# Kernel tuning notes

Measured on AMD Instinct MI355X. Metric: run time of the kernel, lower is better.

The kernel has to match this reference:

```python
import jax, jax.numpy as jnp
import numpy as np
import math

B, S, D = 4, 2048, 1024
WINDOW = 10  # window_size; attends to |i-j| <= WINDOW//2


def setup_inputs() -> dict:
    key = jax.random.key(0)
    ks = jax.random.split(key, 9)
    sc = 1.0 / math.sqrt(D)
    return {
        "x": jax.random.normal(ks[0], (B, S, D), dtype=jnp.float32),
        "Wq": jax.random.normal(ks[1], (D, D), dtype=jnp.float32) * sc,
        "bq": jnp.zeros((D,), dtype=jnp.float32),
        "Wk": jax.random.normal(ks[2], (D, D), dtype=jnp.float32) * sc,
        "bk": jnp.zeros((D,), dtype=jnp.float32),
        "Wv": jax.random.normal(ks[3], (D, D), dtype=jnp.float32) * sc,
        "bv": jnp.zeros((D,), dtype=jnp.float32),
        "Wo": jax.random.normal(ks[4], (D, D), dtype=jnp.float32) * sc,
        "bo": jnp.zeros((D,), dtype=jnp.float32),
    }


def _local_mask(seq_len: int, window_size: int) -> jnp.ndarray:
    # row i attends to columns [i - w//2, i + w//2] inclusive -> |i - j| <= w//2
    i = jnp.arange(seq_len)[:, None]
    j = jnp.arange(seq_len)[None, :]
    return jnp.abs(i - j) <= (window_size // 2)  # [S, S] bool


def reference(x, Wq, bq, Wk, bk, Wv, bv, Wo, bo):
    # nn.Linear: y = x @ W.T + b
    Q = x @ Wq.T + bq  # [B, S, D]
    K = x @ Wk.T + bk
    V = x @ Wv.T + bv
    scores = jnp.einsum("bqd,bkd->bqk", Q, K) / jnp.float32(math.sqrt(D))
    mask = _local_mask(x.shape[1], WINDOW)
    scores = jnp.where(mask[None, :, :], scores, jnp.float32(-1e9))
    attn = jax.nn.softmax(scores, axis=-1)  # [B, S, S]
    context = jnp.einsum("bqk,bkd->bqd", attn, V)
    output = context @ Wo.T + bo
    return output, attn
```

## Files before the change

### kernel.cpp

```cpp
#include <hip/hip_runtime.h>
#include <hip/hip_bf16.h>
#include <cstdint>
#include <cstddef>


typedef __attribute__((ext_vector_type(8))) short bf16x8;
typedef __attribute__((ext_vector_type(4))) float f32x4;
typedef __attribute__((ext_vector_type(8))) unsigned short ushortx8;

#define GPTR(x) ((const __attribute__((address_space(1))) void*)(x))
#define LPTR(x) ((__attribute__((address_space(3))) void*)(x))

__device__ __forceinline__ unsigned short f2bf(float f) {
    __hip_bfloat16 h = __float2bfloat16(f);
    unsigned short u;
    __builtin_memcpy(&u, &h, 2);
    return u;
}
__device__ __forceinline__ float bf2f(unsigned short u) {
    unsigned int x = ((unsigned int)u) << 16;
    float f;
    __builtin_memcpy(&f, &x, 4);
    return f;
}

__global__ void cvt_all(const float* __restrict__ x,
                        const float* __restrict__ Wq, const float* __restrict__ Wk,
                        const float* __restrict__ Wv, const float* __restrict__ Wo,
                        unsigned short* __restrict__ xh,
                        unsigned short* __restrict__ Wcat,
                        unsigned short* __restrict__ Woh) {
    const int idx = blockIdx.x * blockDim.x + threadIdx.x;
    const float* src;
    unsigned short* dst;
    int s_off, d_off;
    if (idx < 2097152) {
        src = x; dst = xh; s_off = idx; d_off = idx;
    } else {
        const int r   = idx - 2097152;
        const int seg = r >> 18;
        const int off = r & 262143;
        src   = (seg == 0) ? Wq : (seg == 1) ? Wk : (seg == 2) ? Wv : Wo;
        dst   = (seg < 3) ? Wcat : Woh;
        s_off = off;
        d_off = (seg < 3) ? (seg << 18) + off : off;
    }
    f32x4 v = reinterpret_cast<const f32x4*>(src)[s_off];
    ushort4 o;
    o.x = f2bf(v[0]); o.y = f2bf(v[1]); o.z = f2bf(v[2]); o.w = f2bf(v[3]);
    reinterpret_cast<ushort4*>(dst)[d_off] = o;
}

__device__ __forceinline__ void gemm_core(const unsigned short* __restrict__ A,
                                          const unsigned short* __restrict__ Bw,
                                          int K, int tm, int tn,
                                          unsigned short* As, unsigned short* Bs,
                                          f32x4 (&acc)[4][4]) {
    const int tid  = threadIdx.x;
    const int lane = tid & 63;
    const int w    = tid >> 6;
    const int wr   = w >> 1;
    const int wc   = w & 1;

    const int lrow8 = lane >> 3;
    const int lcolb = (lane & 7) << 4;

    const char* Abase = (const char*)(A + (size_t)tm * 128 * (size_t)K);
    const char* Bbase = (const char*)(Bw + (size_t)tn * 128 * (size_t)K);
    const size_t rstride = (size_t)K * 2;

    const int nk = K >> 6;
    for (int t = 0; t < nk; ++t) {
        const size_t k0b = ((size_t)t << 6) * 2;
#pragma unroll
        for (int ii = 0; ii < 4; ++ii) {
            const int c    = (w << 2) + ii;
            const int row  = (c << 3) + lrow8;
            const int csrc = lcolb ^ ((row & 7) << 4);
            __builtin_amdgcn_global_load_lds(
                GPTR(Abase + (size_t)row * rstride + k0b + (size_t)csrc),
                LPTR((char*)As + (c << 10)), 16, 0, 0);
            __builtin_amdgcn_global_load_lds(
                GPTR(Bbase + (size_t)row * rstride + k0b + (size_t)csrc),
                LPTR((char*)Bs + (c << 10)), 16, 0, 0);
        }
        __syncthreads();

#pragma unroll
        for (int kk = 0; kk < 2; ++kk) {
            bf16x8 af[4], bfr[4];
            const int cb = (kk << 6) + ((lane >> 4) << 4);
#pragma unroll
            for (int m = 0; m < 4; ++m) {
                const int row = (wr << 6) + (m << 4) + (lane & 15);
                af[m] = *reinterpret_cast<const bf16x8*>(
                    (const char*)As + row * 128 + (cb ^ ((row & 7) << 4)));
            }
#pragma unroll
            for (int n = 0; n < 4; ++n) {
                const int row = (wc << 6) + (n << 4) + (lane & 15);
                bfr[n] = *reinterpret_cast<const bf16x8*>(
                    (const char*)Bs + row * 128 + (cb ^ ((row & 7) << 4)));
            }
#pragma unroll
            for (int m = 0; m < 4; ++m)
#pragma unroll
                for (int n = 0; n < 4; ++n)
                    acc[m][n] = __builtin_amdgcn_mfma_f32_16x16x32_bf16(
                        af[m], bfr[n], acc[m][n], 0, 0, 0);
        }
        __syncthreads();
    }
}

__launch_bounds__(256, 3)
__global__ void gemm_qkv(const unsigned short* __restrict__ A,
                         const unsigned short* __restrict__ Bw,
                         const float* __restrict__ bq, const float* __restrict__ bk,
                         const float* __restrict__ bv,
                         unsigned short* __restrict__ C, int M, int N, int K) {
    __shared__ unsigned short As[128 * 64];
    __shared__ unsigned short Bs[128 * 64];
    f32x4 acc[4][4];
#pragma unroll
    for (int m = 0; m < 4; ++m)
#pragma unroll
        for (int n = 0; n < 4; ++n) acc[m][n] = (f32x4){0.f, 0.f, 0.f, 0.f};

    const int ntn = N >> 7;
    const int sid = (blockIdx.x & 7) * (gridDim.x >> 3) + (blockIdx.x >> 3);
    const int tm  = sid / ntn;
    const int tn  = sid % ntn;

    gemm_core(A, Bw, K, tm, tn, As, Bs, acc);

    const int lane = threadIdx.x & 63;
    const int w    = threadIdx.x >> 6;
    const int wr   = w >> 1, wc = w & 1;
    const int seg  = tn >> 3;
    const float* bp = (seg == 0) ? bq : (seg == 1) ? bk : bv;

    const int col0 = (tn << 7) + (wc << 6) + (lane & 15);
    const int row0 = (tm << 7) + (wr << 6) + ((lane >> 4) << 2);
#pragma unroll
    for (int n = 0; n < 4; ++n) {
        const int col = col0 + (n << 4);
        const float bb = bp[col & 1023];
#pragma unroll
        for (int m = 0; m < 4; ++m) {
            const int row = row0 + (m << 4);
#pragma unroll
            for (int r = 0; r < 4; ++r)
                C[(size_t)(row + r) * (size_t)N + col] = f2bf(acc[m][n][r] + bb);
        }
    }
}

__launch_bounds__(256, 3)
__global__ void gemm_out(const unsigned short* __restrict__ A,
                         const unsigned short* __restrict__ Bw,
                         const float* __restrict__ bias,
                         float* __restrict__ C, int M, int N, int K) {
    __shared__ unsigned short As[128 * 64];
    __shared__ unsigned short Bs[128 * 64];
    f32x4 acc[4][4];
#pragma unroll
    for (int m = 0; m < 4; ++m)
#pragma unroll
        for (int n = 0; n < 4; ++n) acc[m][n] = (f32x4){0.f, 0.f, 0.f, 0.f};

    const int sid = (blockIdx.x & 7) * (gridDim.x >> 3) + (blockIdx.x >> 3);
    const int tm  = sid >> 3;
    const int tn  = sid & 7;

    gemm_core(A, Bw, K, tm, tn, As, Bs, acc);

    const int lane = threadIdx.x & 63;
    const int w    = threadIdx.x >> 6;
    const int wr   = w >> 1, wc = w & 1;
    const int col0 = (tn << 7) + (wc << 6) + (lane & 15);
    const int row0 = (tm << 7) + (wr << 6) + ((lane >> 4) << 2);
#pragma unroll
    for (int n = 0; n < 4; ++n) {
        const int col = col0 + (n << 4);
        const float bb = bias[col];
#pragma unroll
        for (int m = 0; m < 4; ++m) {
            const int row = row0 + (m << 4);
#pragma unroll
            for (int r = 0; r < 4; ++r)
                C[(size_t)(row + r) * (size_t)N + col] = acc[m][n][r] + bb;
        }
    }
}

__launch_bounds__(256, 4)
__global__ void attn_band_kernel(const unsigned short* __restrict__ QKV,
                                 float* __restrict__ attn,
                                 unsigned short* __restrict__ ctx) {
    __shared__ float psm[4][16];
    const int bid  = blockIdx.x;
    const int rb   = (bid & 7) * 256 + (bid >> 3);
    const int w    = threadIdx.x >> 6;
    const int lane = threadIdx.x & 63;
    const int g    = (rb << 2) + w;
    const int b    = g >> 11;
    const int i    = g & 2047;

    const unsigned short* qrow = QKV + (size_t)g * 3072;
    float qf[16];
    {
        ushortx8 qa = *reinterpret_cast<const ushortx8*>(qrow + (lane << 4));
        ushortx8 qb = *reinterpret_cast<const ushortx8*>(qrow + (lane << 4) + 8);
#pragma unroll
        for (int t = 0; t < 8; ++t) { qf[t] = bf2f(qa[t]); qf[8 + t] = bf2f(qb[t]); }
    }

    float s[11];
#pragma unroll
    for (int jj = 0; jj < 11; ++jj) {
        const int j = i - 5 + jj;
        const bool valid = ((unsigned)j < 2048u);
        const int jc = min(max(j, 0), 2047);
        const unsigned short* krow = QKV + ((size_t)(b << 11) + jc) * 3072 + 1024;
        ushortx8 ka = *reinterpret_cast<const ushortx8*>(krow + (lane << 4));
        ushortx8 kb = *reinterpret_cast<const ushortx8*>(krow + (lane << 4) + 8);
        float d = 0.f;
#pragma unroll
        for (int t = 0; t < 8; ++t)
            d += qf[t] * bf2f(ka[t]) + qf[8 + t] * bf2f(kb[t]);
#pragma unroll
        for (int off = 32; off >= 1; off >>= 1) d += __shfl_xor(d, off, 64);
        s[jj] = valid ? d * 0.03125f : -1e30f;
    }

    float mx = s[0];
#pragma unroll
    for (int jj = 1; jj < 11; ++jj) mx = fmaxf(mx, s[jj]);
    float p[11], sum = 0.f;
#pragma unroll
    for (int jj = 0; jj < 11; ++jj) { p[jj] = expf(s[jj] - mx); sum += p[jj]; }
    const float inv = 1.0f / sum;

    if (lane == 0) {
#pragma unroll
        for (int jj = 0; jj < 11; ++jj) psm[w][jj] = p[jj] * inv;
    }
    __syncthreads();

    const int lo = i - 5;
    float* arow = attn + (size_t)g * 2048;
#pragma unroll
    for (int e = 0; e < 8; ++e) {
        const int c0 = (e << 8) + (lane << 2);
        f32x4 v = (f32x4){0.f, 0.f, 0.f, 0.f};
        if (c0 + 3 >= lo && c0 <= lo + 10) {
#pragma unroll
            for (int t = 0; t < 4; ++t) {
                const int d = c0 + t - lo;
                if ((unsigned)d < 11u) v[t] = psm[w][d];
            }
        }
        *reinterpret_cast<f32x4*>(arow + c0) = v;
    }

    float cacc[16];
#pragma unroll
    for (int t = 0; t < 16; ++t) cacc[t] = 0.f;
#pragma unroll
    for (int jj = 0; jj < 11; ++jj) {
        const int j  = i - 5 + jj;
        const int jc = min(max(j, 0), 2047);
        const float pj = p[jj] * inv;
        const unsigned short* vrow = QKV + ((size_t)(b << 11) + jc) * 3072 + 2048;
        ushortx8 va = *reinterpret_cast<const ushortx8*>(vrow + (lane << 4));
        ushortx8 vb = *reinterpret_cast<const ushortx8*>(vrow + (lane << 4) + 8);
#pragma unroll
        for (int t = 0; t < 8; ++t) {
            cacc[t]     += pj * bf2f(va[t]);
            cacc[8 + t] += pj * bf2f(vb[t]);
        }
    }
    unsigned short* cp = ctx + (size_t)g * 1024 + (lane << 4);
    ushortx8 oa, ob;
#pragma unroll
    for (int t = 0; t < 8; ++t) { oa[t] = f2bf(cacc[t]); ob[t] = f2bf(cacc[8 + t]); }
    *reinterpret_cast<ushortx8*>(cp)     = oa;
    *reinterpret_cast<ushortx8*>(cp + 8) = ob;
}

extern "C" void kernel_launch(void* const* d_in, const int* in_sizes, int n_in,
                              void* d_out, int out_size, void* d_ws, size_t ws_size,
                              hipStream_t stream) {
    const float* x  = (const float*)d_in[0];
    const float* Wq = (const float*)d_in[1];
    const float* bq = (const float*)d_in[2];
    const float* Wk = (const float*)d_in[3];
    const float* bk = (const float*)d_in[4];
    const float* Wv = (const float*)d_in[5];
    const float* bv = (const float*)d_in[6];
    const float* Wo = (const float*)d_in[7];
    const float* bo = (const float*)d_in[8];

    const size_t MS = 8192, DD = 1024;

    float* out  = (float*)d_out;
    float* attn = out + MS * DD;

    char* ws = (char*)d_ws;
    unsigned short* xh   = (unsigned short*)ws; ws += MS * DD * 2;
    unsigned short* Wcat = (unsigned short*)ws; ws += 3 * DD * DD * 2;
    unsigned short* Woh  = (unsigned short*)ws; ws += DD * DD * 2;
    unsigned short* QKV  = (unsigned short*)ws; ws += MS * 3 * DD * 2;
    unsigned short* ctx  = (unsigned short*)ws; ws += MS * DD * 2;

    cvt_all<<<dim3(12288), dim3(256), 0, stream>>>(x, Wq, Wk, Wv, Wo, xh, Wcat, Woh);

    gemm_qkv<<<dim3(1536), dim3(256), 0, stream>>>(xh, Wcat, bq, bk, bv,
                                                   QKV, 8192, 3072, 1024);

    attn_band_kernel<<<dim3(2048), dim3(256), 0, stream>>>(QKV, attn, ctx);

    gemm_out<<<dim3(512), dim3(256), 0, stream>>>(ctx, Woh, bo, out, 8192, 1024, 1024);
}
```

Baseline: 136.8 us.

## Fold output projection into V weights by precomputing Wo·Wv

```diff
diff --git a/kernel.cpp b/kernel.cpp
--- a/kernel.cpp
+++ b/kernel.cpp
@@ -26,7 +26,7 @@
 
 __global__ void cvt_all(const float* __restrict__ x,
                         const float* __restrict__ Wq, const float* __restrict__ Wk,
-                        const float* __restrict__ Wv, const float* __restrict__ Wo,
+                        const float* __restrict__ Wo,
                         unsigned short* __restrict__ xh,
                         unsigned short* __restrict__ Wcat,
                         unsigned short* __restrict__ Woh) {
@@ -40,15 +40,50 @@
         const int r   = idx - 2097152;
         const int seg = r >> 18;
         const int off = r & 262143;
-        src   = (seg == 0) ? Wq : (seg == 1) ? Wk : (seg == 2) ? Wv : Wo;
-        dst   = (seg < 3) ? Wcat : Woh;
+        src   = (seg == 0) ? Wq : (seg == 1) ? Wk : Wo;
+        dst   = (seg < 2) ? Wcat : Woh;
         s_off = off;
-        d_off = (seg < 3) ? (seg << 18) + off : off;
+        d_off = (seg < 2) ? (seg << 18) + off : off;
     }
     f32x4 v = reinterpret_cast<const f32x4*>(src)[s_off];
     ushort4 o;
     o.x = f2bf(v[0]); o.y = f2bf(v[1]); o.z = f2bf(v[2]); o.w = f2bf(v[3]);
     reinterpret_cast<ushort4*>(dst)[d_off] = o;
+}
+
+__global__ void transpose_cvt(const float* __restrict__ in,
+                              unsigned short* __restrict__ out) {
+    __shared__ float tl[64][65];
+    const int t  = threadIdx.x;
+    const int c  = t & 63;
+    const int r4 = t >> 6;
+    const int bx = blockIdx.x;
+    const int by = blockIdx.y;
+#pragma unroll
+    for (int i = 0; i < 16; ++i) {
+        const int r = r4 * 16 + i;
+        tl[r][c] = in[(size_t)(by * 64 + r) * 1024 + bx * 64 + c];
+    }
+    __syncthreads();
+#pragma unroll
+    for (int i = 0; i < 16; ++i) {
+        const int r = r4 * 16 + i;
+        out[(size_t)(bx * 64 + r) * 1024 + by * 64 + c] = f2bf(tl[c][r]);
+    }
+}
+
+__global__ void bvo_kernel(const float* __restrict__ Wo,
+                           const float* __restrict__ bv,
+                           float* __restrict__ bvo) {
+    const int row  = blockIdx.x * 4 + (threadIdx.x >> 6);
+    const int lane = threadIdx.x & 63;
+    float s = 0.f;
+#pragma unroll
+    for (int k = lane; k < 1024; k += 64)
+        s += Wo[(size_t)row * 1024 + k] * bv[k];
+#pragma unroll
+    for (int off = 32; off >= 1; off >>= 1) s += __shfl_xor(s, off, 64);
+    if (lane == 0) bvo[row] = s;
 }
 
 __device__ __forceinline__ void gemm_core(const unsigned short* __restrict__ A,
@@ -114,11 +149,9 @@
 }
 
 __launch_bounds__(256, 3)
-__global__ void gemm_qkv(const unsigned short* __restrict__ A,
-                         const unsigned short* __restrict__ Bw,
-                         const float* __restrict__ bq, const float* __restrict__ bk,
-                         const float* __restrict__ bv,
-                         unsigned short* __restrict__ C, int M, int N, int K) {
+__global__ void gemm_wp(const unsigned short* __restrict__ A,
+                        const unsigned short* __restrict__ Bw,
+                        unsigned short* __restrict__ C) {
     __shared__ unsigned short As[128 * 64];
     __shared__ unsigned short Bs[128 * 64];
     f32x4 acc[4][4];
@@ -127,53 +160,11 @@
 #pragma unroll
         for (int n = 0; n < 4; ++n) acc[m][n] = (f32x4){0.f, 0.f, 0.f, 0.f};
 
-    const int ntn = N >> 7;
-    const int sid = (blockIdx.x & 7) * (gridDim.x >> 3) + (blockIdx.x >> 3);
-    const int tm  = sid / ntn;
-    const int tn  = sid % ntn;
-
-    gemm_core(A, Bw, K, tm, tn, As, Bs, acc);
-
-    const int lane = threadIdx.x & 63;
-    const int w    = threadIdx.x >> 6;
-    const int wr   = w >> 1, wc = w & 1;
-    const int seg  = tn >> 3;
-    const float* bp = (seg == 0) ? bq : (seg == 1) ? bk : bv;
-
-    const int col0 = (tn << 7) + (wc << 6) + (lane & 15);
-    const int row0 = (tm << 7) + (wr << 6) + ((lane >> 4) << 2);
-#pragma unroll
-    for (int n = 0; n < 4; ++n) {
-        const int col = col0 + (n << 4);
-        const float bb = bp[col & 1023];
-#pragma unroll
-        for (int m = 0; m < 4; ++m) {
-            const int row = row0 + (m << 4);
-#pragma unroll
-            for (int r = 0; r < 4; ++r)
-                C[(size_t)(row + r) * (size_t)N + col] = f2bf(acc[m][n][r] + bb);
-        }
-    }
-}
-
-__launch_bounds__(256, 3)
-__global__ void gemm_out(const unsigned short* __restrict__ A,
-                         const unsigned short* __restrict__ Bw,
-                         const float* __restrict__ bias,
-                         float* __restrict__ C, int M, int N, int K) {
-    __shared__ unsigned short As[128 * 64];
-    __shared__ unsigned short Bs[128 * 64];
-    f32x4 acc[4][4];
-#pragma unroll
-    for (int m = 0; m < 4; ++m)
-#pragma unroll
-        for (int n = 0; n < 4; ++n) acc[m][n] = (f32x4){0.f, 0.f, 0.f, 0.f};
-
-    const int sid = (blockIdx.x & 7) * (gridDim.x >> 3) + (blockIdx.x >> 3);
+    const int sid = (blockIdx.x & 7) * 8 + (blockIdx.x >> 3);
     const int tm  = sid >> 3;
     const int tn  = sid & 7;
 
-    gemm_core(A, Bw, K, tm, tn, As, Bs, acc);
+    gemm_core(A, Bw, 1024, tm, tn, As, Bs, acc);
 
     const int lane = threadIdx.x & 63;
     const int w    = threadIdx.x >> 6;
@@ -183,21 +174,64 @@
 #pragma unroll
     for (int n = 0; n < 4; ++n) {
         const int col = col0 + (n << 4);
-        const float bb = bias[col];
 #pragma unroll
         for (int m = 0; m < 4; ++m) {
             const int row = row0 + (m << 4);
 #pragma unroll
             for (int r = 0; r < 4; ++r)
-                C[(size_t)(row + r) * (size_t)N + col] = acc[m][n][r] + bb;
+                C[(size_t)(row + r) * 1024 + col] = f2bf(acc[m][n][r]);
+        }
+    }
+}
+
+__launch_bounds__(256, 3)
+__global__ void gemm_qkv(const unsigned short* __restrict__ A,
+                         const unsigned short* __restrict__ Bw,
+                         const float* __restrict__ bq, const float* __restrict__ bk,
+                         const float* __restrict__ bvo,
+                         unsigned short* __restrict__ C, int M, int N, int K) {
+    __shared__ unsigned short As[128 * 64];
+    __shared__ unsigned short Bs[128 * 64];
+    f32x4 acc[4][4];
+#pragma unroll
+    for (int m = 0; m < 4; ++m)
+#pragma unroll
+        for (int n = 0; n < 4; ++n) acc[m][n] = (f32x4){0.f, 0.f, 0.f, 0.f};
+
+    const int ntn = N >> 7;
+    const int sid = (blockIdx.x & 7) * (gridDim.x >> 3) + (blockIdx.x >> 3);
+    const int tm  = sid / ntn;
+    const int tn  = sid % ntn;
+
+    gemm_core(A, Bw, K, tm, tn, As, Bs, acc);
+
+    const int lane = threadIdx.x & 63;
+    const int w    = threadIdx.x >> 6;
+    const int wr   = w >> 1, wc = w & 1;
+    const int seg  = tn >> 3;
+    const float* bp = (seg == 0) ? bq : (seg == 1) ? bk : bvo;
+
+    const int col0 = (tn << 7) + (wc << 6) + (lane & 15);
+    const int row0 = (tm << 7) + (wr << 6) + ((lane >> 4) << 2);
+#pragma unroll
+    for (int n = 0; n < 4; ++n) {
+        const int col = col0 + (n << 4);
+        const float bb = bp[col & 1023];
+#pragma unroll
+        for (int m = 0; m < 4; ++m) {
+            const int row = row0 + (m << 4);
+#pragma unroll
+            for (int r = 0; r < 4; ++r)
+                C[(size_t)(row + r) * (size_t)N + col] = f2bf(acc[m][n][r] + bb);
         }
     }
 }
 
 __launch_bounds__(256, 4)
 __global__ void attn_band_kernel(const unsigned short* __restrict__ QKV,
+                                 const float* __restrict__ bo,
                                  float* __restrict__ attn,
-                                 unsigned short* __restrict__ ctx) {
+                                 float* __restrict__ outp) {
     __shared__ float psm[4][16];
     const int bid  = blockIdx.x;
     const int rb   = (bid & 7) * 256 + (bid >> 3);
@@ -281,12 +315,16 @@
             cacc[8 + t] += pj * bf2f(vb[t]);
         }
     }
-    unsigned short* cp = ctx + (size_t)g * 1024 + (lane << 4);
-    ushortx8 oa, ob;
-#pragma unroll
-    for (int t = 0; t < 8; ++t) { oa[t] = f2bf(cacc[t]); ob[t] = f2bf(cacc[8 + t]); }
-    *reinterpret_cast<ushortx8*>(cp)     = oa;
-    *reinterpret_cast<ushortx8*>(cp + 8) = ob;
+    const int c0 = lane << 4;
+    float* op = outp + (size_t)g * 1024 + c0;
+#pragma unroll
+    for (int q = 0; q < 4; ++q) {
+        f32x4 bb = *reinterpret_cast<const f32x4*>(bo + c0 + (q << 2));
+        f32x4 o;
+#pragma unroll
+        for (int t = 0; t < 4; ++t) o[t] = cacc[(q << 2) + t] + bb[t];
+        *reinterpret_cast<f32x4*>(op + (q << 2)) = o;
+    }
 }
 
 extern "C" void kernel_launch(void* const* d_in, const int* in_sizes, int n_in,
@@ -311,15 +349,18 @@
     unsigned short* xh   = (unsigned short*)ws; ws += MS * DD * 2;
     unsigned short* Wcat = (unsigned short*)ws; ws += 3 * DD * DD * 2;
     unsigned short* Woh  = (unsigned short*)ws; ws += DD * DD * 2;
+    unsigned short* Wvt  = (unsigned short*)ws; ws += DD * DD * 2;
+    float*          bvo  = (float*)ws;          ws += DD * 4;
     unsigned short* QKV  = (unsigned short*)ws; ws += MS * 3 * DD * 2;
-    unsigned short* ctx  = (unsigned short*)ws; ws += MS * DD * 2;
-
-    cvt_all<<<dim3(12288), dim3(256), 0, stream>>>(x, Wq, Wk, Wv, Wo, xh, Wcat, Woh);
-
-    gemm_qkv<<<dim3(1536), dim3(256), 0, stream>>>(xh, Wcat, bq, bk, bv,
+
+    bvo_kernel<<<dim3(256), dim3(256), 0, stream>>>(Wo, bv, bvo);
+    transpose_cvt<<<dim3(16, 16), dim3(256), 0, stream>>>(Wv, Wvt);
+    cvt_all<<<dim3(11264), dim3(256), 0, stream>>>(x, Wq, Wk, Wo, xh, Wcat, Woh);
+
+    gemm_wp<<<dim3(64), dim3(256), 0, stream>>>(Woh, Wvt, Wcat + 2 * DD * DD);
+
+    gemm_qkv<<<dim3(1536), dim3(256), 0, stream>>>(xh, Wcat, bq, bk, bvo,
                                                    QKV, 8192, 3072, 1024);
 
-    attn_band_kernel<<<dim3(2048), dim3(256), 0, stream>>>(QKV, attn, ctx);
-
-    gemm_out<<<dim3(512), dim3(256), 0, stream>>>(ctx, Woh, bo, out, 8192, 1024, 1024);
-}
+    attn_band_kernel<<<dim3(2048), dim3(256), 0, stream>>>(QKV, bo, attn, out);
+}
```

New measurement: 132.8 us. -2.9%, faster.
